# Optimization experiments

Hardware: AMD Instinct MI355X
Metric: run time of the kernel (lower is better)

Reference implementation:

```python
import jax, jax.numpy as jnp
import numpy as np

ROPE_BASE = 10000.0

def _rms_norm(x):
    eps = jnp.asarray(jnp.finfo(x.dtype).eps, x.dtype)
    return x * jax.lax.rsqrt(jnp.mean(x * x, axis=-1, keepdims=True) + eps)

def _rope(x):
    # x: [B, S, H, hd]; rotate-halves variant: y1 = x1*cos + x2*sin, y2 = -x1*sin + x2*cos
    S, hd = x.shape[1], x.shape[3]
    d = hd // 2
    inv_freq = 1.0 / (ROPE_BASE ** (jnp.arange(0, hd, 2, dtype=jnp.float32) / hd))  # [d]
    t = jnp.arange(S, dtype=jnp.float32)
    freqs = jnp.outer(t, inv_freq)                       # [S, d]
    cos = jnp.cos(freqs)[None, :, None, :].astype(x.dtype)
    sin = jnp.sin(freqs)[None, :, None, :].astype(x.dtype)
    x1, x2 = x[..., :d], x[..., d:]
    return jnp.concatenate([x1 * cos + x2 * sin, -x1 * sin + x2 * cos], axis=-1)

def setup_inputs() -> dict:
    key = jax.random.key(0)
    ks = jax.random.split(key, 7)
    B, S, D = 1, 2048, 1024
    std = 0.02
    return {
        "x": jax.random.normal(ks[0], (B, S, D), jnp.float32),
        "v1": jax.random.normal(ks[1], (B, S, D), jnp.float32),
        "Wq": jax.random.normal(ks[2], (D, D), jnp.float32) * std,
        "Wk": jax.random.normal(ks[3], (D, D), jnp.float32) * std,
        "Wv": jax.random.normal(ks[4], (D, D), jnp.float32) * std,
        "Wout": jax.random.normal(ks[5], (D, D), jnp.float32) * std,
        "lambdas": jnp.float32(0.5),
        "n_heads": 16,
    }

def reference(x, v1, Wq, Wk, Wv, Wout, lambdas, n_heads):
    B, S, D = x.shape
    H = n_heads
    hd = D // H
    # QKV projections (CastedLinear, no bias)
    q = (x @ Wq.T).reshape(B, S, H, hd)
    k = (x @ Wk.T).reshape(B, S, H, hd)
    v = (x @ Wv.T).reshape(B, S, H, hd)
    # value residual mix with first-layer values v1
    v = (1.0 - lambdas) * v + lambdas * v1.reshape(B, S, H, hd)
    # per-head RMS norm (no learned scale) then RoPE
    q, k = _rms_norm(q), _rms_norm(k)
    q, k = _rope(q), _rope(k)
    # causal attention (flex_attention default: softmax, scale 1/sqrt(hd))
    scale = 1.0 / jnp.sqrt(jnp.asarray(hd, x.dtype))
    scores = jnp.einsum('bqhd,bkhd->bhqk', q, k) * scale        # [B,H,S,S]
    causal = jnp.tril(jnp.ones((S, S), dtype=bool))
    scores = jnp.where(causal[None, None], scores, jnp.asarray(-jnp.inf, scores.dtype))
    p = jax.nn.softmax(scores, axis=-1)
    y = jnp.einsum('bhqk,bkhd->bqhd', p, v).reshape(B, S, D)
    y = y @ Wout.T
    return (y, v1)
```

## Files before the change

### kernel.cpp

```cpp
#include <hip/hip_runtime.h>
#include <hip/hip_bf16.h>

#define S_LEN 2048
#define D_DIM 1024
#define NH    16
#define NEG_BIG (-1.0e30f)

#define EPI_NORMROPE   1
#define EPI_VMIX_T     2
#define EPI_F32        3
#define EPI_NORMROPE_Q 4

typedef __attribute__((ext_vector_type(8))) short bf16x8;
typedef __attribute__((ext_vector_type(4))) float f32x4;
typedef const __attribute__((address_space(1))) unsigned char gu8_t;
typedef __attribute__((address_space(3))) unsigned char lu8_t;

__device__ __forceinline__ float bf2f(unsigned short h) {
    union { unsigned int u; float f; } v; v.u = ((unsigned int)h) << 16; return v.f;
}
__device__ __forceinline__ unsigned short f2b(float f) {
    union { float f; unsigned int u; } v; v.f = f;
    unsigned int u = v.u;
    return (unsigned short)((u + 0x7FFFu + ((u >> 16) & 1u)) >> 16);
}
__device__ __forceinline__ unsigned short f2b_trunc(float f) {
    union { float f; unsigned int u; } v; v.f = f;
    return (unsigned short)(v.u >> 16);
}

__global__ __launch_bounds__(256)
void to_bf16(const float* __restrict__ x,  const float* __restrict__ wq,
             const float* __restrict__ wk, const float* __restrict__ wv,
             const float* __restrict__ wo,
             unsigned short* __restrict__ xb,  unsigned short* __restrict__ wqb,
             unsigned short* __restrict__ wkb, unsigned short* __restrict__ wvb,
             unsigned short* __restrict__ wob)
{
    const int z = blockIdx.y;
    const float* s; unsigned short* d; int n;
    switch (z) {
        case 0: s = x;  d = xb;  n = S_LEN * D_DIM; break;
        case 1: s = wq; d = wqb; n = D_DIM * D_DIM; break;
        case 2: s = wk; d = wkb; n = D_DIM * D_DIM; break;
        case 3: s = wv; d = wvb; n = D_DIM * D_DIM; break;
        default: s = wo; d = wob; n = D_DIM * D_DIM; break;
    }
    int i8 = blockIdx.x * 256 + threadIdx.x;
    if (i8 * 8 >= n) return;
    const float* sp = s + (size_t)i8 * 8;
    float4 lo = *(const float4*)sp, hi = *(const float4*)(sp + 4);
    uint4 p;
    p.x = f2b(lo.x) | ((unsigned)f2b(lo.y) << 16);
    p.y = f2b(lo.z) | ((unsigned)f2b(lo.w) << 16);
    p.z = f2b(hi.x) | ((unsigned)f2b(hi.y) << 16);
    p.w = f2b(hi.z) | ((unsigned)f2b(hi.w) << 16);
    *(uint4*)(d + (size_t)i8 * 8) = p;
}

__global__ __launch_bounds__(256, 3)
void gemm_bt(const unsigned short* __restrict__ A,
             const unsigned short* __restrict__ B0, const unsigned short* __restrict__ B1,
             const unsigned short* __restrict__ B2,
             void* __restrict__ C0, void* __restrict__ C1, void* __restrict__ C2,
             const float* __restrict__ vmix, const float* __restrict__ lam,
             int epiPack)
{
    const int which = blockIdx.z;
    const unsigned short* Bp = (which == 0) ? B0 : ((which == 1) ? B1 : B2);
    void* C = (which == 0) ? C0 : ((which == 1) ? C1 : C2);
    const int epi = (epiPack >> (8 * which)) & 0xff;
    const int tn = blockIdx.x * 128;
    const int tm = blockIdx.y * 128;

    __shared__ unsigned short Asl[128 * 32];
    __shared__ unsigned short Bsl[128 * 32];

    const int t    = threadIdx.x;
    const int lane = t & 63;
    const int wave = t >> 6;
    const int wm   = (wave >> 1) * 64;
    const int wn   = (wave & 1) * 64;
    const int lrow = lane & 15;
    const int quad = lane >> 4;
    const int srow = lane >> 2;
    const int scol = (lane & 3) * 8;

    f32x4 acc[4][4];
    #pragma unroll
    for (int i = 0; i < 4; ++i)
        #pragma unroll
        for (int j = 0; j < 4; ++j) {
            f32x4 z = {0.f, 0.f, 0.f, 0.f};
            acc[i][j] = z;
        }

    for (int k0 = 0; k0 < D_DIM; k0 += 32) {
        #pragma unroll
        for (int rep = 0; rep < 2; ++rep) {
            int grp = wave * 2 + rep;
            int row = grp * 16 + srow;
            __builtin_amdgcn_global_load_lds(
                (gu8_t*)(A + (size_t)(tm + row) * D_DIM + k0 + scol),
                (lu8_t*)&Asl[grp * 512], 16, 0, 0);
            __builtin_amdgcn_global_load_lds(
                (gu8_t*)(Bp + (size_t)(tn + row) * D_DIM + k0 + scol),
                (lu8_t*)&Bsl[grp * 512], 16, 0, 0);
        }
        __syncthreads();
        bf16x8 af[4], bfr[4];
        #pragma unroll
        for (int i = 0; i < 4; ++i)
            af[i] = *(const bf16x8*)(&Asl[(wm + i * 16 + lrow) * 32 + quad * 8]);
        #pragma unroll
        for (int j = 0; j < 4; ++j)
            bfr[j] = *(const bf16x8*)(&Bsl[(wn + j * 16 + lrow) * 32 + quad * 8]);
        #pragma unroll
        for (int i = 0; i < 4; ++i)
            #pragma unroll
            for (int j = 0; j < 4; ++j)
                acc[i][j] = __builtin_amdgcn_mfma_f32_16x16x32_bf16(af[i], bfr[j], acc[i][j], 0, 0, 0);
        __syncthreads();
    }

    if (epi == EPI_NORMROPE || epi == EPI_NORMROPE_Q) {
        const float post = (epi == EPI_NORMROPE_Q) ? 0.18033688011112042f : 1.0f;
        #pragma unroll
        for (int i = 0; i < 4; ++i) {
            #pragma unroll
            for (int r = 0; r < 4; ++r) {
                int row = tm + wm + i * 16 + quad * 4 + r;
                float v0 = acc[i][0][r], v1 = acc[i][1][r];
                float v2 = acc[i][2][r], v3 = acc[i][3][r];
                float ss = v0 * v0 + v1 * v1 + v2 * v2 + v3 * v3;
                ss += __shfl_xor(ss, 1); ss += __shfl_xor(ss, 2);
                ss += __shfl_xor(ss, 4); ss += __shfl_xor(ss, 8);
                float rms = rsqrtf(ss * (1.f / 64.f) + 1.1920929e-7f) * post;
                v0 *= rms; v1 *= rms; v2 *= rms; v3 *= rms;
                float fs = (float)row;
                float a0 = fs * exp2f(-0.41524101186092030f * (float)lrow);
                float a1 = fs * exp2f(-0.41524101186092030f * (float)(16 + lrow));
                float s0, c0, s1, c1;
                __sincosf(a0, &s0, &c0);
                __sincosf(a1, &s1, &c1);
                unsigned short* Cb = (unsigned short*)C;
                size_t base = (size_t)row * D_DIM + tn + wn + lrow;
                Cb[base]      = f2b(v0 * c0 + v2 * s0);
                Cb[base + 16] = f2b(v1 * c1 + v3 * s1);
                Cb[base + 32] = f2b(-v0 * s0 + v2 * c0);
                Cb[base + 48] = f2b(-v1 * s1 + v3 * c1);
            }
        }
    } else if (epi == EPI_VMIX_T) {
        float lamf = *lam;
        #pragma unroll
        for (int i = 0; i < 4; ++i) {
            int cm0 = tm + wm + i * 16 + quad * 4;
            #pragma unroll
            for (int j = 0; j < 4; ++j) {
                int cn = tn + wn + j * 16 + lrow;
                ushort4 pk;
                float vals[4];
                #pragma unroll
                for (int r = 0; r < 4; ++r) {
                    size_t idx = (size_t)(cm0 + r) * D_DIM + cn;
                    vals[r] = (1.f - lamf) * acc[i][j][r] + lamf * vmix[idx];
                }
                pk.x = f2b(vals[0]); pk.y = f2b(vals[1]);
                pk.z = f2b(vals[2]); pk.w = f2b(vals[3]);
                *(ushort4*)((unsigned short*)C + (size_t)cn * S_LEN + cm0) = pk;
            }
        }
    } else {
        #pragma unroll
        for (int i = 0; i < 4; ++i) {
            int cm0 = tm + wm + i * 16 + quad * 4;
            #pragma unroll
            for (int j = 0; j < 4; ++j) {
                int cn = tn + wn + j * 16 + lrow;
                #pragma unroll
                for (int r = 0; r < 4; ++r)
                    ((float*)C)[(size_t)(cm0 + r) * D_DIM + cn] = acc[i][j][r];
            }
        }
    }
}

__global__ __launch_bounds__(256, 2)
void attn_mfma(const unsigned short* Qb,
               const unsigned short* __restrict__ Kb,
               const unsigned short* __restrict__ Vtg,
               unsigned short* Ob)
{
    const int bx = blockIdx.x;
    const int qt = (bx & 1) ? (31 - (bx >> 1)) : (bx >> 1);
    const int h  = blockIdx.y;
    const int t  = threadIdx.x;
    const int w  = t >> 6;
    const int l  = t & 63;
    const int l15  = l & 15;
    const int quad = l >> 4;
    const int hco  = h * 64;

    __shared__ unsigned short Ks[2][64][72];
    __shared__ unsigned short Vt[2][64][72];
    __shared__ unsigned short Ps[4][16][72];

    const unsigned short* qrow = Qb + (size_t)(qt * 64 + w * 16 + l15) * D_DIM + hco;
    bf16x8 qf0 = *(const bf16x8*)(qrow + quad * 8);
    bf16x8 qf1 = *(const bf16x8*)(qrow + 32 + quad * 8);

    f32x4 oac[4];
    #pragma unroll
    for (int nt = 0; nt < 4; ++nt) { f32x4 z = {0.f,0.f,0.f,0.f}; oac[nt] = z; }
    float l_lane[4] = {0.f, 0.f, 0.f, 0.f};

    const int rr = t >> 2;
    const int dc = (t & 3) * 16;

    const unsigned short* kbase = Kb  + (size_t)rr * D_DIM + hco + dc;
    const unsigned short* vbase = Vtg + (size_t)(hco + rr) * S_LEN + dc;

    uint4 ka0, ka1, va0, va1;
    ka0 = *(const uint4*)kbase;  ka1 = *(const uint4*)(kbase + 8);
    va0 = *(const uint4*)vbase;  va1 = *(const uint4*)(vbase + 8);

    const int row_base = qt * 64 + w * 16 + quad * 4;
    const float C2 = -11.541560327111707f;

    for (int j = 0; j <= qt; ++j) {
        const int buf = j & 1;
        *(uint4*)&Ks[buf][rr][dc]     = ka0;
        *(uint4*)&Ks[buf][rr][dc + 8] = ka1;
        *(uint4*)&Vt[buf][rr][dc]     = va0;
        *(uint4*)&Vt[buf][rr][dc + 8] = va1;
        __syncthreads();
        if (j < qt) {
            const unsigned short* kp = kbase + (size_t)(j + 1) * 64 * D_DIM;
            const unsigned short* vp = vbase + (size_t)(j + 1) * 64;
            ka0 = *(const uint4*)kp;  ka1 = *(const uint4*)(kp + 8);
            va0 = *(const uint4*)vp;  va1 = *(const uint4*)(vp + 8);
        }

        f32x4 sac[4];
        #pragma unroll
        for (int nt = 0; nt < 4; ++nt) {
            f32x4 z = {0.f,0.f,0.f,0.f};
            bf16x8 kf0 = *(const bf16x8*)&Ks[buf][nt * 16 + l15][quad * 8];
            z = __builtin_amdgcn_mfma_f32_16x16x32_bf16(qf0, kf0, z, 0, 0, 0);
            bf16x8 kf1 = *(const bf16x8*)&Ks[buf][nt * 16 + l15][32 + quad * 8];
            z = __builtin_amdgcn_mfma_f32_16x16x32_bf16(qf1, kf1, z, 0, 0, 0);
            sac[nt] = z;
        }

        if (j < qt) {
            #pragma unroll
            for (int nt = 0; nt < 4; ++nt) {
                #pragma unroll
                for (int r = 0; r < 4; ++r) {
                    float pe = exp2f(sac[nt][r] + C2);
                    l_lane[r] += pe;
                    Ps[w][quad * 4 + r][nt * 16 + l15] = f2b_trunc(pe);
                }
            }
        } else {
            #pragma unroll
            for (int nt = 0; nt < 4; ++nt) {
                int key_g = j * 64 + nt * 16 + l15;
                #pragma unroll
                for (int r = 0; r < 4; ++r) {
                    float s = sac[nt][r] + C2;
                    if (key_g > row_base + r) s = NEG_BIG;
                    float pe = exp2f(s);
                    l_lane[r] += pe;
                    Ps[w][quad * 4 + r][nt * 16 + l15] = f2b_trunc(pe);
                }
            }
        }

        bf16x8 pf0 = *(const bf16x8*)&Ps[w][l15][quad * 8];
        bf16x8 pf1 = *(const bf16x8*)&Ps[w][l15][32 + quad * 8];
        #pragma unroll
        for (int nt = 0; nt < 4; ++nt) {
            bf16x8 vf0 = *(const bf16x8*)&Vt[buf][nt * 16 + l15][quad * 8];
            oac[nt] = __builtin_amdgcn_mfma_f32_16x16x32_bf16(pf0, vf0, oac[nt], 0, 0, 0);
            bf16x8 vf1 = *(const bf16x8*)&Vt[buf][nt * 16 + l15][32 + quad * 8];
            oac[nt] = __builtin_amdgcn_mfma_f32_16x16x32_bf16(pf1, vf1, oac[nt], 0, 0, 0);
        }
    }

    float inv[4];
    #pragma unroll
    for (int r = 0; r < 4; ++r) {
        float lr = l_lane[r];
        #pragma unroll
        for (int d = 1; d < 16; d <<= 1) lr += __shfl_xor(lr, d);
        inv[r] = 1.f / lr;
    }
    #pragma unroll
    for (int nt = 0; nt < 4; ++nt) {
        #pragma unroll
        for (int r = 0; r < 4; ++r) {
            int row_g = row_base + r;
            Ob[(size_t)row_g * D_DIM + hco + nt * 16 + l15] = f2b(oac[nt][r] * inv[r]);
        }
    }
}

__global__ __launch_bounds__(256)
void copy_v1(const uint4* __restrict__ src, uint4* __restrict__ dst) {
    int i = blockIdx.x * 256 + threadIdx.x;
    dst[i] = src[i];
}

extern "C" void kernel_launch(void* const* d_in, const int* in_sizes, int n_in,
                              void* d_out, int out_size, void* d_ws, size_t ws_size,
                              hipStream_t stream)
{
    const float* x    = (const float*)d_in[0];
    const float* v1   = (const float*)d_in[1];
    const float* Wq   = (const float*)d_in[2];
    const float* Wk   = (const float*)d_in[3];
    const float* Wv   = (const float*)d_in[4];
    const float* Wout = (const float*)d_in[5];
    const float* lam  = (const float*)d_in[6];
    float* out = (float*)d_out;

    const size_t SD = (size_t)S_LEN * D_DIM;
    const size_t DD = (size_t)D_DIM * D_DIM;
    unsigned short* Qb  = (unsigned short*)d_ws;
    unsigned short* Kb  = Qb + SD;
    unsigned short* Vtg = Kb + SD;
    unsigned short* Ab  = Qb;

    unsigned short* Wqb   = (unsigned short*)d_out;
    unsigned short* Wkb   = Wqb + DD;
    unsigned short* Wvb   = Wkb + DD;
    unsigned short* xb    = (unsigned short*)(out + SD);
    unsigned short* Woutb = xb + SD;

    to_bf16<<<dim3(1024, 5), 256, 0, stream>>>(
        x, Wq, Wk, Wv, Wout, xb, Wqb, Wkb, Wvb, Woutb);

    gemm_bt<<<dim3(D_DIM / 128, S_LEN / 128, 3), 256, 0, stream>>>(
        xb, Wqb, Wkb, Wvb, Qb, Kb, Vtg, v1, lam,
        EPI_NORMROPE_Q | (EPI_NORMROPE << 8) | (EPI_VMIX_T << 16));

    attn_mfma<<<dim3(S_LEN / 64, NH), 256, 0, stream>>>(Qb, Kb, Vtg, Ab);

    gemm_bt<<<dim3(D_DIM / 128, S_LEN / 128, 1), 256, 0, stream>>>(
        Ab, Woutb, Woutb, Woutb, d_out, d_out, d_out, nullptr, lam, EPI_F32);

    copy_v1<<<dim3((unsigned)(SD / 4 / 256)), 256, 0, stream>>>(
        (const uint4*)v1, (uint4*)(out + SD));
}
```

Before: 181.1 us.

## Split causal attention KV range into four chunks with a separate combine kernel

Each query tile's causal key range is split into up to four chunks, each handled by its own block. Blocks write unnormalized fp32 partial outputs and row sums to workspace, and a new combine kernel adds them, normalizes and writes bf16. This is meant to shorten the critical path set by the longest causal tiles and to expose more blocks; launch bounds also rise to three blocks per CU. In exchange it adds an extra kernel launch, extra fp32 partial traffic to and from workspace, and needs a larger workspace.

```diff
diff --git a/kernel.cpp b/kernel.cpp
--- a/kernel.cpp
+++ b/kernel.cpp
@@ -186,14 +186,19 @@
     }
 }
 
-__global__ __launch_bounds__(256, 2)
+__global__ __launch_bounds__(256, 3)
 void attn_mfma(const unsigned short* Qb,
                const unsigned short* __restrict__ Kb,
                const unsigned short* __restrict__ Vtg,
-               unsigned short* Ob)
+               float* __restrict__ Opart, float* __restrict__ Lpart)
 {
     const int bx = blockIdx.x;
-    const int qt = (bx & 1) ? (31 - (bx >> 1)) : (bx >> 1);
+    const int qt = 31 - (bx >> 2);
+    const int c  = bx & 3;
+    const int cs = (qt + 4) >> 2;
+    const int jlo = c * cs;
+    if (jlo > qt) return;
+    const int jhi = min(jlo + cs - 1, qt);
     const int h  = blockIdx.y;
     const int t  = threadIdx.x;
     const int w  = t >> 6;
@@ -201,6 +206,7 @@
     const int l15  = l & 15;
     const int quad = l >> 4;
     const int hco  = h * 64;
+    const int slot = (qt * 4 + c) * NH + h;
 
     __shared__ unsigned short Ks[2][64][72];
     __shared__ unsigned short Vt[2][64][72];
@@ -222,20 +228,24 @@
     const unsigned short* vbase = Vtg + (size_t)(hco + rr) * S_LEN + dc;
 
     uint4 ka0, ka1, va0, va1;
-    ka0 = *(const uint4*)kbase;  ka1 = *(const uint4*)(kbase + 8);
-    va0 = *(const uint4*)vbase;  va1 = *(const uint4*)(vbase + 8);
+    {
+        const unsigned short* kp = kbase + (size_t)jlo * 64 * D_DIM;
+        const unsigned short* vp = vbase + (size_t)jlo * 64;
+        ka0 = *(const uint4*)kp;  ka1 = *(const uint4*)(kp + 8);
+        va0 = *(const uint4*)vp;  va1 = *(const uint4*)(vp + 8);
+    }
 
     const int row_base = qt * 64 + w * 16 + quad * 4;
     const float C2 = -11.541560327111707f;
 
-    for (int j = 0; j <= qt; ++j) {
-        const int buf = j & 1;
+    for (int j = jlo; j <= jhi; ++j) {
+        const int buf = (j - jlo) & 1;
         *(uint4*)&Ks[buf][rr][dc]     = ka0;
         *(uint4*)&Ks[buf][rr][dc + 8] = ka1;
         *(uint4*)&Vt[buf][rr][dc]     = va0;
         *(uint4*)&Vt[buf][rr][dc + 8] = va1;
         __syncthreads();
-        if (j < qt) {
+        if (j < jhi) {
             const unsigned short* kp = kbase + (size_t)(j + 1) * 64 * D_DIM;
             const unsigned short* vp = vbase + (size_t)(j + 1) * 64;
             ka0 = *(const uint4*)kp;  ka1 = *(const uint4*)(kp + 8);
@@ -289,22 +299,55 @@
         }
     }
 
-    float inv[4];
+    float* Op = Opart + (size_t)slot * 4096;
     #pragma unroll
     for (int r = 0; r < 4; ++r) {
         float lr = l_lane[r];
         #pragma unroll
         for (int d = 1; d < 16; d <<= 1) lr += __shfl_xor(lr, d);
-        inv[r] = 1.f / lr;
-    }
-    #pragma unroll
-    for (int nt = 0; nt < 4; ++nt) {
-        #pragma unroll
-        for (int r = 0; r < 4; ++r) {
-            int row_g = row_base + r;
-            Ob[(size_t)row_g * D_DIM + hco + nt * 16 + l15] = f2b(oac[nt][r] * inv[r]);
-        }
-    }
+        if (l15 == 0) Lpart[(size_t)slot * 64 + w * 16 + quad * 4 + r] = lr;
+    }
+    #pragma unroll
+    for (int nt = 0; nt < 4; ++nt)
+        #pragma unroll
+        for (int r = 0; r < 4; ++r)
+            Op[(size_t)(w * 16 + quad * 4 + r) * 64 + nt * 16 + l15] = oac[nt][r];
+}
+
+__global__ __launch_bounds__(256)
+void attn_combine(const float* __restrict__ Opart, const float* __restrict__ Lpart,
+                  unsigned short* __restrict__ Ob)
+{
+    const int qt  = blockIdx.x;
+    const int h   = blockIdx.y;
+    const int t   = threadIdx.x;
+    const int row = t >> 2;
+    const int c0  = (t & 3) * 16;
+    const int cs  = (qt + 4) >> 2;
+    float acc[16];
+    #pragma unroll
+    for (int i = 0; i < 16; ++i) acc[i] = 0.f;
+    float lsum = 0.f;
+    for (int c = 0; c < 4; ++c) {
+        if (c * cs > qt) break;
+        const size_t slot = (size_t)((qt * 4 + c) * NH + h);
+        const float* Op = Opart + slot * 4096 + (size_t)row * 64 + c0;
+        #pragma unroll
+        for (int g = 0; g < 4; ++g) {
+            float4 a = *(const float4*)(Op + g * 4);
+            acc[g * 4 + 0] += a.x; acc[g * 4 + 1] += a.y;
+            acc[g * 4 + 2] += a.z; acc[g * 4 + 3] += a.w;
+        }
+        lsum += Lpart[slot * 64 + row];
+    }
+    const float inv = 1.f / lsum;
+    unsigned int pk[8];
+    #pragma unroll
+    for (int i = 0; i < 8; ++i)
+        pk[i] = f2b(acc[2 * i] * inv) | ((unsigned)f2b(acc[2 * i + 1] * inv) << 16);
+    unsigned short* dst = Ob + (size_t)(qt * 64 + row) * D_DIM + h * 64 + c0;
+    *(uint4*)dst       = make_uint4(pk[0], pk[1], pk[2], pk[3]);
+    *(uint4*)(dst + 8) = make_uint4(pk[4], pk[5], pk[6], pk[7]);
 }
 
 __global__ __launch_bounds__(256)
@@ -332,6 +375,8 @@
     unsigned short* Kb  = Qb + SD;
     unsigned short* Vtg = Kb + SD;
     unsigned short* Ab  = Qb;
+    float* Opart = (float*)(Vtg + SD);
+    float* Lpart = Opart + (size_t)2048 * 4096;
 
     unsigned short* Wqb   = (unsigned short*)d_out;
     unsigned short* Wkb   = Wqb + DD;
@@ -346,7 +391,8 @@
         xb, Wqb, Wkb, Wvb, Qb, Kb, Vtg, v1, lam,
         EPI_NORMROPE_Q | (EPI_NORMROPE << 8) | (EPI_VMIX_T << 16));
 
-    attn_mfma<<<dim3(S_LEN / 64, NH), 256, 0, stream>>>(Qb, Kb, Vtg, Ab);
+    attn_mfma<<<dim3(128, NH), 256, 0, stream>>>(Qb, Kb, Vtg, Opart, Lpart);
+    attn_combine<<<dim3(S_LEN / 64, NH), 256, 0, stream>>>(Opart, Lpart, Ab);
 
     gemm_bt<<<dim3(D_DIM / 128, S_LEN / 128, 1), 256, 0, stream>>>(
         Ab, Woutb, Woutb, Woutb, d_out, d_out, d_out, nullptr, lam, EPI_F32);
```

After: 181.5 us. No clear change (+0.2%).
